# Performance work log

Measured on AMD Instinct MI355X. Metric: run time of the kernel, lower is better.

Reference implementation:

```python
import jax, jax.numpy as jnp
import numpy as np

B, NA, NB, DIM = 1024, 48, 24, 680  # batch, res_alpha(=res_gamma), res_beta, irreps dim = sum_{l<=7}(2l+1)^2


def setup_inputs() -> dict:
    key = jax.random.key(0)
    k1, k2, k3 = jax.random.split(key, 3)
    features = jax.random.normal(k1, (B, DIM), dtype=jnp.float32)
    D = jax.random.normal(k2, (NA, NB, NA, DIM), dtype=jnp.float32)  # stands in for the precomputed Wigner-D buffer
    qw = jax.random.uniform(k3, (NB,), dtype=jnp.float32)  # quadrature weights over beta
    return {"features": features, "D": D, "qw": qw}


def reference(features, D, qw):
    dim = D.shape[-1]
    scale = float(np.sqrt(dim))
    # to_grid: '...i,abci->...abc' / sqrt(dim)
    grid = jnp.einsum('ni,abci->nabc', features, D) / scale  # (B, na, nb, na)
    # from_grid: '...abc,abci,b->...i' * sqrt(dim)  (qw contracts the beta axis)
    out = jnp.einsum('nabc,abci,b->ni', grid, D, qw) * scale  # (B, dim)
    return out
```

## Files before the change

kernel.cpp:

```cpp
#include <hip/hip_runtime.h>
#include <stdint.h>

#define DIM    680
#define DPAD   768
#define NCH    864
#define NB_Q   24
#define SPLITS 36
#define STAGES 24
#define NTILE  6

typedef __bf16 bf16x8 __attribute__((ext_vector_type(8)));
typedef float  f32x16 __attribute__((ext_vector_type(16)));

typedef __attribute__((address_space(3))) unsigned       lds_u32;
typedef __attribute__((address_space(1))) const unsigned glb_u32;

__constant__ int c_tj[NTILE] = {0, 0, 0, 1, 1, 2};
__constant__ int c_ti[NTILE] = {0, 1, 2, 1, 2, 2};

static __device__ __forceinline__ unsigned f2bf(float x) {
    union { float f; unsigned u; } c; c.f = x;
    unsigned u = c.u;
    return (u + 0x7FFFu + ((u >> 16) & 1u)) >> 16;
}

static __device__ __forceinline__ float bf2f(unsigned short h) {
    union { unsigned u; float f; } c; c.u = ((unsigned)h) << 16;
    return c.f;
}

__global__ __launch_bounds__(256) void k1_transpose(
        const float* __restrict__ D, const float* __restrict__ qw,
        uint4* __restrict__ awt) {
    __shared__ float sq[NB_Q];
    __shared__ float tile[4096];
    const int t   = threadIdx.x;
    const int cg0 = blockIdx.x * 4;
    const int i0  = blockIdx.y * 64;
    if (t < NB_Q) sq[t] = sqrtf(qw[t]);

    int  rowr[4], gcol[4];
    bool inb[4];
#pragma unroll
    for (int rd = 0; rd < 4; ++rd) {
        const int row = rd * 16 + (t >> 4);
        const int p   = row >> 3;
        const int sg  = (t & 15) ^ p;
        rowr[rd] = row;
        gcol[rd] = i0 + sg * 4;
        inb[rd]  = (gcol[rd] < DIM);
        if (!inb[rd]) {
            float4 z = {0.f, 0.f, 0.f, 0.f};
            *reinterpret_cast<float4*>(&tile[rd * 1024 + t * 4]) = z;
        }
    }
    __syncthreads();

    for (int cc = 0; cc < 4; ++cc) {
        const int cg = cg0 + cc;
        const int g0 = cg * 64;
#pragma unroll
        for (int rd = 0; rd < 4; ++rd) {
            if (inb[rd]) {
                __builtin_amdgcn_global_load_lds(
                    (glb_u32*)(D + (size_t)(g0 + rowr[rd]) * DIM + gcol[rd]),
                    (lds_u32*)(&tile[rd * 1024 + t * 4]), 16, 0, 0);
            }
        }
        __syncthreads();

#pragma unroll
        for (int s = 0; s < 2; ++s) {
            const int l  = t + s * 256;
            const int c  = l >> 3;
            const int kc = l & 7;
            unsigned h[8];
#pragma unroll
            for (int j = 0; j < 8; ++j) {
                const int row = kc * 8 + j;
                const float v = tile[row * 64 + (((c >> 2) ^ kc) << 2) + (c & 3)];
                const int b = ((g0 + row) / 48) % 24;
                h[j] = f2bf(v * sq[b]);
            }
            uint4 o;
            o.x = h[0] | (h[1] << 16);
            o.y = h[2] | (h[3] << 16);
            o.z = h[4] | (h[5] << 16);
            o.w = h[6] | (h[7] << 16);
            const size_t slot = ((size_t)cg * DPAD + (size_t)(i0 + c)) * 8
                              + (size_t)(kc ^ (c & 7));
            awt[slot] = o;
        }
        __syncthreads();
    }
}

__global__ __launch_bounds__(256) void kf_conv(const float* __restrict__ F,
                                               uint4* __restrict__ Fb) {
    const int idx = blockIdx.x * 256 + threadIdx.x;
    const int row = idx / 96;
    const int c0  = (idx % 96) * 8;
    uint4 o = {0u, 0u, 0u, 0u};
    if (c0 < DIM) {
        const float4 a = *reinterpret_cast<const float4*>(F + (size_t)row * DIM + c0);
        const float4 b = *reinterpret_cast<const float4*>(F + (size_t)row * DIM + c0 + 4);
        o.x = f2bf(a.x) | (f2bf(a.y) << 16);
        o.y = f2bf(a.z) | (f2bf(a.w) << 16);
        o.z = f2bf(b.x) | (f2bf(b.y) << 16);
        o.w = f2bf(b.z) | (f2bf(b.w) << 16);
    }
    Fb[idx] = o;
}

__global__ __launch_bounds__(512) void k2_gram(const uint4* __restrict__ awt,
                                               uint2* __restrict__ parts) {
    __shared__ uint4 smA[2][2048];
    __shared__ uint4 smB[2][2048];
    const int t  = threadIdx.x;
    const int h       = blockIdx.x;
    const int logical = (h & 7) * 27 + (h >> 3);
    const int split   = logical / 6;
    const int t6      = logical % 6;
    const int tj    = c_tj[t6];
    const int ti    = c_ti[t6];
    const bool diag = (tj == ti);
    const int wave  = t >> 6;
    const int lane  = t & 63;
    const int wm    = wave & 3;
    const int wn    = wave >> 2;
    const int cl    = lane & 31;
    const int half  = lane >> 5;

    f32x16 acc[2][4];
    const f32x16 zero = {};
#pragma unroll
    for (int a = 0; a < 2; ++a)
#pragma unroll
        for (int b = 0; b < 4; ++b) acc[a][b] = zero;

#define K2_STAGE(st_, buf_)                                                   \
    do {                                                                      \
        const int    cg_ = split * STAGES + (st_);                            \
        const size_t bA_ = ((size_t)cg_ * DPAD + tj * 256) * 8;               \
        _Pragma("unroll")                                                     \
        for (int j = 0; j < 4; ++j) {                                         \
            __builtin_amdgcn_global_load_lds(                                 \
                (glb_u32*)(awt + bA_ + j * 512 + t),                          \
                (lds_u32*)(&smA[(buf_)][j * 512 + t]), 16, 0, 0);             \
        }                                                                     \
        if (!diag) {                                                          \
            const size_t bB_ = ((size_t)cg_ * DPAD + ti * 256) * 8;           \
            _Pragma("unroll")                                                 \
            for (int j = 0; j < 4; ++j) {                                     \
                __builtin_amdgcn_global_load_lds(                             \
                    (glb_u32*)(awt + bB_ + j * 512 + t),                      \
                    (lds_u32*)(&smB[(buf_)][j * 512 + t]), 16, 0, 0);         \
            }                                                                 \
        }                                                                     \
    } while (0)

    K2_STAGE(0, 0);
    __syncthreads();

    for (int st = 0; st < STAGES; ++st) {
        const int cur = st & 1;
        if (st + 1 < STAGES) K2_STAGE(st + 1, cur ^ 1);

        const bf16x8* pA = reinterpret_cast<const bf16x8*>(smA[cur]);
        const bf16x8* pB = diag ? pA : reinterpret_cast<const bf16x8*>(smB[cur]);
#pragma unroll
        for (int t4 = 0; t4 < 4; ++t4) {
            const int kc = 2 * t4 + half;
            bf16x8 af[2], bfr[4];
#pragma unroll
            for (int ms = 0; ms < 2; ++ms) {
                const int col = wm * 64 + ms * 32 + cl;
                af[ms] = pA[col * 8 + (kc ^ (col & 7))];
            }
#pragma unroll
            for (int ns = 0; ns < 4; ++ns) {
                const int col = wn * 128 + ns * 32 + cl;
                bfr[ns] = pB[col * 8 + (kc ^ (col & 7))];
            }
#pragma unroll
            for (int ms = 0; ms < 2; ++ms)
#pragma unroll
                for (int ns = 0; ns < 4; ++ns)
                    acc[ms][ns] = __builtin_amdgcn_mfma_f32_32x32x16_bf16(
                        af[ms], bfr[ns], acc[ms][ns], 0, 0, 0);
        }
        __syncthreads();
    }
#undef K2_STAGE

    uint2* pt = parts + (size_t)(split * NTILE + t6) * 16384;
#pragma unroll
    for (int ms = 0; ms < 2; ++ms) {
        const int rowb = wm * 64 + ms * 32 + 4 * half;
#pragma unroll
        for (int ns = 0; ns < 4; ++ns) {
            const int colt = wn * 128 + ns * 32 + cl;
#pragma unroll
            for (int q = 0; q < 4; ++q) {
                uint2 w;
                w.x = f2bf(acc[ms][ns][q * 4 + 0]) | (f2bf(acc[ms][ns][q * 4 + 1]) << 16);
                w.y = f2bf(acc[ms][ns][q * 4 + 2]) | (f2bf(acc[ms][ns][q * 4 + 3]) << 16);
                pt[(size_t)(((rowb >> 2) + 2 * q) * 256 + colt)] = w;
            }
        }
    }
}

__global__ __launch_bounds__(256) void k2_reduce(
        const uint2* __restrict__ parts, unsigned short* __restrict__ Mb) {
    const int t6 = blockIdx.y;
    const int tj = c_tj[t6];
    const int ti = c_ti[t6];
    const int idx4 = blockIdx.x * 256 + threadIdx.x;
    const int w0 = idx4 * 2;
    const int quad = w0 >> 8;
    const int c = w0 & 255;
    float s[8] = {0.f, 0.f, 0.f, 0.f, 0.f, 0.f, 0.f, 0.f};
    const uint4* base = reinterpret_cast<const uint4*>(parts) + idx4;
#pragma unroll 4
    for (int sp = 0; sp < SPLITS; ++sp) {
        const uint4 u = base[(size_t)(sp * NTILE + t6) * 8192];
        s[0] += bf2f((unsigned short)(u.x & 0xFFFF));
        s[1] += bf2f((unsigned short)(u.x >> 16));
        s[2] += bf2f((unsigned short)(u.y & 0xFFFF));
        s[3] += bf2f((unsigned short)(u.y >> 16));
        s[4] += bf2f((unsigned short)(u.z & 0xFFFF));
        s[5] += bf2f((unsigned short)(u.z >> 16));
        s[6] += bf2f((unsigned short)(u.w & 0xFFFF));
        s[7] += bf2f((unsigned short)(u.w >> 16));
    }
    const int R = tj * 256 + 4 * quad;
    const int C = ti * 256 + c;
#pragma unroll
    for (int i = 0; i < 4; ++i) {
        const unsigned w = f2bf(s[i]) | (f2bf(s[4 + i]) << 16);
        *reinterpret_cast<unsigned*>(Mb + (size_t)(R + i) * DPAD + C) = w;
    }
    if (ti != tj) {
        uint2 m0, m1;
        m0.x = f2bf(s[0]) | (f2bf(s[1]) << 16);
        m0.y = f2bf(s[2]) | (f2bf(s[3]) << 16);
        m1.x = f2bf(s[4]) | (f2bf(s[5]) << 16);
        m1.y = f2bf(s[6]) | (f2bf(s[7]) << 16);
        *reinterpret_cast<uint2*>(Mb + (size_t)(C + 0) * DPAD + R) = m0;
        *reinterpret_cast<uint2*>(Mb + (size_t)(C + 1) * DPAD + R) = m1;
    }
}

__global__ __launch_bounds__(64) void k3_mfma(const uint4* __restrict__ Fb,
                                              const uint4* __restrict__ Mb,
                                              float* __restrict__ out) {
    __shared__ uint4 sA[2][512];
    __shared__ uint4 sB[2][512];
    const int t    = threadIdx.x;
    const int n0   = blockIdx.x * 64;
    const int i0   = blockIdx.y * 64;
    const int cl   = t & 31;
    const int half = t >> 5;

    f32x16 acc[2][2];
    const f32x16 zero = {};
    acc[0][0] = zero; acc[0][1] = zero; acc[1][0] = zero; acc[1][1] = zero;

#define K3_STAGE(ck_, buf_)                                                   \
    do {                                                                      \
        const int kcs_ = t & 7;                                               \
        _Pragma("unroll")                                                     \
        for (int j = 0; j < 8; ++j) {                                         \
            const int nl_ = j * 8 + (t >> 3);                                 \
            const int sc_ = (ck_) * 8 + (kcs_ ^ (nl_ & 7));                   \
            __builtin_amdgcn_global_load_lds(                                 \
                (glb_u32*)(Fb + (size_t)(n0 + nl_) * 96 + sc_),               \
                (lds_u32*)(&sA[(buf_)][j * 64 + t]), 16, 0, 0);               \
            __builtin_amdgcn_global_load_lds(                                 \
                (glb_u32*)(Mb + (size_t)(i0 + nl_) * 96 + sc_),               \
                (lds_u32*)(&sB[(buf_)][j * 64 + t]), 16, 0, 0);               \
        }                                                                     \
    } while (0)

    K3_STAGE(0, 0);
    asm volatile("s_waitcnt vmcnt(0)" ::: "memory");

    for (int ck = 0; ck < 12; ++ck) {
        const int cur = ck & 1;
        if (ck + 1 < 12) {
            asm volatile("s_waitcnt lgkmcnt(0)" ::: "memory");
            K3_STAGE(ck + 1, cur ^ 1);
            asm volatile("s_waitcnt vmcnt(16)" ::: "memory");
        }
        const bf16x8* pA = reinterpret_cast<const bf16x8*>(sA[cur]);
        const bf16x8* pB = reinterpret_cast<const bf16x8*>(sB[cur]);
#pragma unroll
        for (int t4 = 0; t4 < 4; ++t4) {
            const int kc = 2 * t4 + half;
            bf16x8 af[2], bv[2];
#pragma unroll
            for (int ms = 0; ms < 2; ++ms) {
                const int col = ms * 32 + cl;
                af[ms] = pA[col * 8 + (kc ^ (col & 7))];
            }
#pragma unroll
            for (int ns = 0; ns < 2; ++ns) {
                const int col = ns * 32 + cl;
                bv[ns] = pB[col * 8 + (kc ^ (col & 7))];
            }
#pragma unroll
            for (int ms = 0; ms < 2; ++ms)
#pragma unroll
                for (int ns = 0; ns < 2; ++ns)
                    acc[ms][ns] = __builtin_amdgcn_mfma_f32_32x32x16_bf16(
                        af[ms], bv[ns], acc[ms][ns], 0, 0, 0);
        }
    }
#undef K3_STAGE

#pragma unroll
    for (int ms = 0; ms < 2; ++ms) {
        const int rowb = ms * 32 + 4 * half;
#pragma unroll
        for (int ns = 0; ns < 2; ++ns) {
            const int col = i0 + ns * 32 + cl;
            if (col < DIM) {
#pragma unroll
                for (int q = 0; q < 4; ++q)
#pragma unroll
                    for (int j = 0; j < 4; ++j)
                        out[(size_t)(n0 + rowb + 8 * q + j) * DIM + col]
                            = acc[ms][ns][4 * q + j];
            }
        }
    }
}

extern "C" void kernel_launch(void* const* d_in, const int* in_sizes, int n_in,
                              void* d_out, int out_size, void* d_ws, size_t ws_size,
                              hipStream_t stream) {
    const float* F  = (const float*)d_in[0];
    const float* D  = (const float*)d_in[1];
    const float* qw = (const float*)d_in[2];
    float* out = (float*)d_out;
    char*  ws  = (char*)d_ws;

    uint4* awt = (uint4*)ws;
    const size_t awt_bytes = (size_t)NCH * DPAD * 64 * 2;
    uint2* parts = (uint2*)(ws + awt_bytes);
    const size_t parts_bytes = (size_t)SPLITS * NTILE * 16384 * 8;
    unsigned short* Mb = (unsigned short*)(ws + awt_bytes + parts_bytes);
    const size_t mb_bytes = (size_t)DPAD * DPAD * 2;
    uint4* Fb = (uint4*)(ws + awt_bytes + parts_bytes + mb_bytes);

    k1_transpose<<<dim3(NCH / 4, DPAD / 64), 256, 0, stream>>>(D, qw, awt);
    kf_conv<<<dim3(1024 * DPAD / 8 / 256), 256, 0, stream>>>(F, Fb);
    k2_gram<<<dim3(SPLITS * NTILE), 512, 0, stream>>>(awt, parts);
    k2_reduce<<<dim3(32, NTILE), 256, 0, stream>>>(parts, Mb);
    k3_mfma<<<dim3(16, 11), 64, 0, stream>>>(Fb, (const uint4*)Mb, out);
}
```

Baseline: 303.5 us.

## Double-buffer transpose loads and deepen GEMM prefetch with explicit vmcnt waits

The transpose kernel now uses two LDS tiles, so the global-to-LDS load for the next chunk is issued while the current one is converted, and one barrier per iteration is removed. The GEMM kernel prefetches two stages ahead and replaces __syncthreads with manual s_waitcnt vmcnt counts plus raw s_barrier, so loads stay in flight across iterations. It also raises wave priority around the MFMA block. The hand-tuned vmcnt values must exactly match the number of outstanding loads per stage, so any change to the load count would silently break correctness.

```diff
diff --git a/kernel.cpp b/kernel.cpp
--- a/kernel.cpp
+++ b/kernel.cpp
@@ -33,7 +33,7 @@
         const float* __restrict__ D, const float* __restrict__ qw,
         uint4* __restrict__ awt) {
     __shared__ float sq[NB_Q];
-    __shared__ float tile[4096];
+    __shared__ float tile[2][4096];
     const int t   = threadIdx.x;
     const int cg0 = blockIdx.x * 4;
     const int i0  = blockIdx.y * 64;
@@ -51,23 +51,33 @@
         inb[rd]  = (gcol[rd] < DIM);
         if (!inb[rd]) {
             float4 z = {0.f, 0.f, 0.f, 0.f};
-            *reinterpret_cast<float4*>(&tile[rd * 1024 + t * 4]) = z;
-        }
-    }
+            *reinterpret_cast<float4*>(&tile[0][rd * 1024 + t * 4]) = z;
+            *reinterpret_cast<float4*>(&tile[1][rd * 1024 + t * 4]) = z;
+        }
+    }
+
+#define K1_STAGE(cc_, buf_)                                                   \
+    do {                                                                      \
+        const int g0_ = (cg0 + (cc_)) * 64;                                   \
+        _Pragma("unroll")                                                     \
+        for (int rd = 0; rd < 4; ++rd) {                                      \
+            if (inb[rd]) {                                                    \
+                __builtin_amdgcn_global_load_lds(                             \
+                    (glb_u32*)(D + (size_t)(g0_ + rowr[rd]) * DIM + gcol[rd]),\
+                    (lds_u32*)(&tile[(buf_)][rd * 1024 + t * 4]), 16, 0, 0);  \
+            }                                                                 \
+        }                                                                     \
+    } while (0)
+
     __syncthreads();
+    K1_STAGE(0, 0);
 
     for (int cc = 0; cc < 4; ++cc) {
-        const int cg = cg0 + cc;
-        const int g0 = cg * 64;
-#pragma unroll
-        for (int rd = 0; rd < 4; ++rd) {
-            if (inb[rd]) {
-                __builtin_amdgcn_global_load_lds(
-                    (glb_u32*)(D + (size_t)(g0 + rowr[rd]) * DIM + gcol[rd]),
-                    (lds_u32*)(&tile[rd * 1024 + t * 4]), 16, 0, 0);
-            }
-        }
+        const int cur = cc & 1;
+        const int cg  = cg0 + cc;
+        const int g0  = cg * 64;
         __syncthreads();
+        if (cc + 1 < 4) K1_STAGE(cc + 1, cur ^ 1);
 
 #pragma unroll
         for (int s = 0; s < 2; ++s) {
@@ -78,7 +88,7 @@
 #pragma unroll
             for (int j = 0; j < 8; ++j) {
                 const int row = kc * 8 + j;
-                const float v = tile[row * 64 + (((c >> 2) ^ kc) << 2) + (c & 3)];
+                const float v = tile[cur][row * 64 + (((c >> 2) ^ kc) << 2) + (c & 3)];
                 const int b = ((g0 + row) / 48) % 24;
                 h[j] = f2bf(v * sq[b]);
             }
@@ -91,8 +101,8 @@
                               + (size_t)(kc ^ (c & 7));
             awt[slot] = o;
         }
-        __syncthreads();
-    }
+    }
+#undef K1_STAGE
 }
 
 __global__ __launch_bounds__(256) void kf_conv(const float* __restrict__ F,
@@ -160,11 +170,17 @@
     } while (0)
 
     K2_STAGE(0, 0);
-    __syncthreads();
+    K2_STAGE(1, 1);
 
     for (int st = 0; st < STAGES; ++st) {
         const int cur = st & 1;
-        if (st + 1 < STAGES) K2_STAGE(st + 1, cur ^ 1);
+        if (st + 1 < STAGES) {
+            if (diag) asm volatile("s_waitcnt vmcnt(4)" ::: "memory");
+            else      asm volatile("s_waitcnt vmcnt(8)" ::: "memory");
+        } else {
+            asm volatile("s_waitcnt vmcnt(0)" ::: "memory");
+        }
+        __builtin_amdgcn_s_barrier();
 
         const bf16x8* pA = reinterpret_cast<const bf16x8*>(smA[cur]);
         const bf16x8* pB = diag ? pA : reinterpret_cast<const bf16x8*>(smB[cur]);
@@ -182,14 +198,18 @@
                 const int col = wn * 128 + ns * 32 + cl;
                 bfr[ns] = pB[col * 8 + (kc ^ (col & 7))];
             }
+            __builtin_amdgcn_s_setprio(1);
 #pragma unroll
             for (int ms = 0; ms < 2; ++ms)
 #pragma unroll
                 for (int ns = 0; ns < 4; ++ns)
                     acc[ms][ns] = __builtin_amdgcn_mfma_f32_32x32x16_bf16(
                         af[ms], bfr[ns], acc[ms][ns], 0, 0, 0);
-        }
-        __syncthreads();
+            __builtin_amdgcn_s_setprio(0);
+        }
+        asm volatile("s_waitcnt lgkmcnt(0)" ::: "memory");
+        __builtin_amdgcn_s_barrier();
+        if (st + 2 < STAGES) K2_STAGE(st + 2, cur);
     }
 #undef K2_STAGE
 
```

Measured after the change: 306.9 us. No clear change (+1.1%).

## Fuse D transpose/convert into gram kernel with register-staged prefetch

Applied to the files above, without the earlier changes.

Removes the separate transpose kernel and the bf16 intermediate buffer by having the gram kernel load fp32 D directly into registers, scale by sqrt(qw), convert to bf16 and write swizzled tiles into LDS. Next-stage global loads are issued into registers before the MFMA compute, replacing double-buffered async LDS loads with a single LDS buffer. It also adds s_setprio around the MFMA block. The trade-off is that D is re-read from global memory by several tiles and register pressure increases.

```diff
diff --git a/kernel.cpp b/kernel.cpp
--- a/kernel.cpp
+++ b/kernel.cpp
@@ -3,7 +3,6 @@
 
 #define DIM    680
 #define DPAD   768
-#define NCH    864
 #define NB_Q   24
 #define SPLITS 36
 #define STAGES 24
@@ -29,69 +28,139 @@
     return c.f;
 }
 
-__global__ __launch_bounds__(256) void k1_transpose(
-        const float* __restrict__ D, const float* __restrict__ qw,
-        uint4* __restrict__ awt) {
+__global__ __launch_bounds__(512) void k12_gram(const float* __restrict__ D,
+                                                const float* __restrict__ qw,
+                                                uint2* __restrict__ parts) {
     __shared__ float sq[NB_Q];
-    __shared__ float tile[4096];
-    const int t   = threadIdx.x;
-    const int cg0 = blockIdx.x * 4;
-    const int i0  = blockIdx.y * 64;
+    __shared__ uint4 smA[2048];
+    __shared__ uint4 smB[2048];
+    const int t  = threadIdx.x;
+    const int h       = blockIdx.x;
+    const int logical = (h & 7) * 27 + (h >> 3);
+    const int split   = logical / 6;
+    const int t6      = logical % 6;
+    const int tj    = c_tj[t6];
+    const int ti    = c_ti[t6];
+    const bool diag = (tj == ti);
+    const int cl_ = t & 255;
+    const int hg  = t >> 8;
+    const int cA  = tj * 256 + cl_;
+    const int cB  = ti * 256 + cl_;
+    const bool vA = (cA < DIM);
+    const bool vB = (cB < DIM);
+    const int cAc = vA ? cA : (DIM - 1);
+    const int cBc = vB ? cB : (DIM - 1);
+    const int wave  = t >> 6;
+    const int lane  = t & 63;
+    const int wm    = wave & 3;
+    const int wn    = wave >> 2;
+    const int cl    = lane & 31;
+    const int half  = lane >> 5;
+
+    f32x16 acc[2][4];
+    const f32x16 zero = {};
+#pragma unroll
+    for (int a = 0; a < 2; ++a)
+#pragma unroll
+        for (int b = 0; b < 4; ++b) acc[a][b] = zero;
+
+    float ra[32], rb[32];
+
+#define K12_LOAD(reg_, st_, csrc_)                                            \
+    do {                                                                      \
+        const int g0_ = (split * STAGES + (st_)) * 64 + hg * 32;              \
+        _Pragma("unroll")                                                     \
+        for (int u_ = 0; u_ < 32; ++u_)                                       \
+            reg_[u_] = D[(size_t)(g0_ + u_) * DIM + (csrc_)];                 \
+    } while (0)
+
+#define K12_CONV(reg_, valid_, sm_, st_)                                      \
+    do {                                                                      \
+        const int gg_ = (split * STAGES + (st_)) * 64 + hg * 32;              \
+        _Pragma("unroll")                                                     \
+        for (int kcg_ = 0; kcg_ < 4; ++kcg_) {                                \
+            const int G_ = gg_ + kcg_ * 8;                                    \
+            const int q_ = G_ / 48;                                           \
+            const int r_ = G_ - q_ * 48;                                      \
+            const float s0_ = sq[q_ % 24];                                    \
+            const float s1_ = sq[(q_ + 1) % 24];                              \
+            unsigned hh_[8];                                                  \
+            _Pragma("unroll")                                                 \
+            for (int j_ = 0; j_ < 8; ++j_) {                                  \
+                const float sc_ = (r_ + j_ < 48) ? s0_ : s1_;                 \
+                hh_[j_] = (valid_) ? f2bf(reg_[kcg_ * 8 + j_] * sc_) : 0u;    \
+            }                                                                 \
+            uint4 o_;                                                         \
+            o_.x = hh_[0] | (hh_[1] << 16);                                   \
+            o_.y = hh_[2] | (hh_[3] << 16);                                   \
+            o_.z = hh_[4] | (hh_[5] << 16);                                   \
+            o_.w = hh_[6] | (hh_[7] << 16);                                   \
+            sm_[cl_ * 8 + ((hg * 4 + kcg_) ^ (cl_ & 7))] = o_;                \
+        }                                                                     \
+    } while (0)
+
+    K12_LOAD(ra, 0, cAc);
+    if (!diag) K12_LOAD(rb, 0, cBc);
     if (t < NB_Q) sq[t] = sqrtf(qw[t]);
-
-    int  rowr[4], gcol[4];
-    bool inb[4];
-#pragma unroll
-    for (int rd = 0; rd < 4; ++rd) {
-        const int row = rd * 16 + (t >> 4);
-        const int p   = row >> 3;
-        const int sg  = (t & 15) ^ p;
-        rowr[rd] = row;
-        gcol[rd] = i0 + sg * 4;
-        inb[rd]  = (gcol[rd] < DIM);
-        if (!inb[rd]) {
-            float4 z = {0.f, 0.f, 0.f, 0.f};
-            *reinterpret_cast<float4*>(&tile[rd * 1024 + t * 4]) = z;
-        }
-    }
-    __syncthreads();
-
-    for (int cc = 0; cc < 4; ++cc) {
-        const int cg = cg0 + cc;
-        const int g0 = cg * 64;
-#pragma unroll
-        for (int rd = 0; rd < 4; ++rd) {
-            if (inb[rd]) {
-                __builtin_amdgcn_global_load_lds(
-                    (glb_u32*)(D + (size_t)(g0 + rowr[rd]) * DIM + gcol[rd]),
-                    (lds_u32*)(&tile[rd * 1024 + t * 4]), 16, 0, 0);
-            }
-        }
-        __syncthreads();
-
-#pragma unroll
-        for (int s = 0; s < 2; ++s) {
-            const int l  = t + s * 256;
-            const int c  = l >> 3;
-            const int kc = l & 7;
-            unsigned h[8];
-#pragma unroll
-            for (int j = 0; j < 8; ++j) {
-                const int row = kc * 8 + j;
-                const float v = tile[row * 64 + (((c >> 2) ^ kc) << 2) + (c & 3)];
-                const int b = ((g0 + row) / 48) % 24;
-                h[j] = f2bf(v * sq[b]);
-            }
-            uint4 o;
-            o.x = h[0] | (h[1] << 16);
-            o.y = h[2] | (h[3] << 16);
-            o.z = h[4] | (h[5] << 16);
-            o.w = h[6] | (h[7] << 16);
-            const size_t slot = ((size_t)cg * DPAD + (size_t)(i0 + c)) * 8
-                              + (size_t)(kc ^ (c & 7));
-            awt[slot] = o;
-        }
-        __syncthreads();
+    asm volatile("s_waitcnt lgkmcnt(0)" ::: "memory");
+    __builtin_amdgcn_s_barrier();
+
+    for (int st = 0; st < STAGES; ++st) {
+        K12_CONV(ra, vA, smA, st);
+        if (st + 1 < STAGES) K12_LOAD(ra, st + 1, cAc);
+        if (!diag) {
+            K12_CONV(rb, vB, smB, st);
+            if (st + 1 < STAGES) K12_LOAD(rb, st + 1, cBc);
+        }
+        asm volatile("s_waitcnt lgkmcnt(0)" ::: "memory");
+        __builtin_amdgcn_s_barrier();
+
+        const bf16x8* pA = reinterpret_cast<const bf16x8*>(smA);
+        const bf16x8* pB = diag ? pA : reinterpret_cast<const bf16x8*>(smB);
+#pragma unroll
+        for (int t4 = 0; t4 < 4; ++t4) {
+            const int kc = 2 * t4 + half;
+            bf16x8 af[2], bfr[4];
+#pragma unroll
+            for (int ms = 0; ms < 2; ++ms) {
+                const int col = wm * 64 + ms * 32 + cl;
+                af[ms] = pA[col * 8 + (kc ^ (col & 7))];
+            }
+#pragma unroll
+            for (int ns = 0; ns < 4; ++ns) {
+                const int col = wn * 128 + ns * 32 + cl;
+                bfr[ns] = pB[col * 8 + (kc ^ (col & 7))];
+            }
+            __builtin_amdgcn_s_setprio(1);
+#pragma unroll
+            for (int ms = 0; ms < 2; ++ms)
+#pragma unroll
+                for (int ns = 0; ns < 4; ++ns)
+                    acc[ms][ns] = __builtin_amdgcn_mfma_f32_32x32x16_bf16(
+                        af[ms], bfr[ns], acc[ms][ns], 0, 0, 0);
+            __builtin_amdgcn_s_setprio(0);
+        }
+        asm volatile("s_waitcnt lgkmcnt(0)" ::: "memory");
+        __builtin_amdgcn_s_barrier();
+    }
+#undef K12_LOAD
+#undef K12_CONV
+
+    uint2* pt = parts + (size_t)(split * NTILE + t6) * 16384;
+#pragma unroll
+    for (int ms = 0; ms < 2; ++ms) {
+        const int rowb = wm * 64 + ms * 32 + 4 * half;
+#pragma unroll
+        for (int ns = 0; ns < 4; ++ns) {
+            const int colt = wn * 128 + ns * 32 + cl;
+#pragma unroll
+            for (int q = 0; q < 4; ++q) {
+                uint2 w;
+                w.x = f2bf(acc[ms][ns][q * 4 + 0]) | (f2bf(acc[ms][ns][q * 4 + 1]) << 16);
+                w.y = f2bf(acc[ms][ns][q * 4 + 2]) | (f2bf(acc[ms][ns][q * 4 + 3]) << 16);
+                pt[(size_t)(((rowb >> 2) + 2 * q) * 256 + colt)] = w;
+            }
+        }
     }
 }
 
@@ -110,105 +179,6 @@
         o.w = f2bf(b.z) | (f2bf(b.w) << 16);
     }
     Fb[idx] = o;
-}
-
-__global__ __launch_bounds__(512) void k2_gram(const uint4* __restrict__ awt,
-                                               uint2* __restrict__ parts) {
-    __shared__ uint4 smA[2][2048];
-    __shared__ uint4 smB[2][2048];
-    const int t  = threadIdx.x;
-    const int h       = blockIdx.x;
-    const int logical = (h & 7) * 27 + (h >> 3);
-    const int split   = logical / 6;
-    const int t6      = logical % 6;
-    const int tj    = c_tj[t6];
-    const int ti    = c_ti[t6];
-    const bool diag = (tj == ti);
-    const int wave  = t >> 6;
-    const int lane  = t & 63;
-    const int wm    = wave & 3;
-    const int wn    = wave >> 2;
-    const int cl    = lane & 31;
-    const int half  = lane >> 5;
-
-    f32x16 acc[2][4];
-    const f32x16 zero = {};
-#pragma unroll
-    for (int a = 0; a < 2; ++a)
-#pragma unroll
-        for (int b = 0; b < 4; ++b) acc[a][b] = zero;
-
-#define K2_STAGE(st_, buf_)                                                   \
-    do {                                                                      \
-        const int    cg_ = split * STAGES + (st_);                            \
-        const size_t bA_ = ((size_t)cg_ * DPAD + tj * 256) * 8;               \
-        _Pragma("unroll")                                                     \
-        for (int j = 0; j < 4; ++j) {                                         \
-            __builtin_amdgcn_global_load_lds(                                 \
-                (glb_u32*)(awt + bA_ + j * 512 + t),                          \
-                (lds_u32*)(&smA[(buf_)][j * 512 + t]), 16, 0, 0);             \
-        }                                                                     \
-        if (!diag) {                                                          \
-            const size_t bB_ = ((size_t)cg_ * DPAD + ti * 256) * 8;           \
-            _Pragma("unroll")                                                 \
-            for (int j = 0; j < 4; ++j) {                                     \
-                __builtin_amdgcn_global_load_lds(                             \
-                    (glb_u32*)(awt + bB_ + j * 512 + t),                      \
-                    (lds_u32*)(&smB[(buf_)][j * 512 + t]), 16, 0, 0);         \
-            }                                                                 \
-        }                                                                     \
-    } while (0)
-
-    K2_STAGE(0, 0);
-    __syncthreads();
-
-    for (int st = 0; st < STAGES; ++st) {
-        const int cur = st & 1;
-        if (st + 1 < STAGES) K2_STAGE(st + 1, cur ^ 1);
-
-        const bf16x8* pA = reinterpret_cast<const bf16x8*>(smA[cur]);
-        const bf16x8* pB = diag ? pA : reinterpret_cast<const bf16x8*>(smB[cur]);
-#pragma unroll
-        for (int t4 = 0; t4 < 4; ++t4) {
-            const int kc = 2 * t4 + half;
-            bf16x8 af[2], bfr[4];
-#pragma unroll
-            for (int ms = 0; ms < 2; ++ms) {
-                const int col = wm * 64 + ms * 32 + cl;
-                af[ms] = pA[col * 8 + (kc ^ (col & 7))];
-            }
-#pragma unroll
-            for (int ns = 0; ns < 4; ++ns) {
-                const int col = wn * 128 + ns * 32 + cl;
-                bfr[ns] = pB[col * 8 + (kc ^ (col & 7))];
-            }
-#pragma unroll
-            for (int ms = 0; ms < 2; ++ms)
-#pragma unroll
-                for (int ns = 0; ns < 4; ++ns)
-                    acc[ms][ns] = __builtin_amdgcn_mfma_f32_32x32x16_bf16(
-                        af[ms], bfr[ns], acc[ms][ns], 0, 0, 0);
-        }
-        __syncthreads();
-    }
-#undef K2_STAGE
-
-    uint2* pt = parts + (size_t)(split * NTILE + t6) * 16384;
-#pragma unroll
-    for (int ms = 0; ms < 2; ++ms) {
-        const int rowb = wm * 64 + ms * 32 + 4 * half;
-#pragma unroll
-        for (int ns = 0; ns < 4; ++ns) {
-            const int colt = wn * 128 + ns * 32 + cl;
-#pragma unroll
-            for (int q = 0; q < 4; ++q) {
-                uint2 w;
-                w.x = f2bf(acc[ms][ns][q * 4 + 0]) | (f2bf(acc[ms][ns][q * 4 + 1]) << 16);
-                w.y = f2bf(acc[ms][ns][q * 4 + 2]) | (f2bf(acc[ms][ns][q * 4 + 3]) << 16);
-                pt[(size_t)(((rowb >> 2) + 2 * q) * 256 + colt)] = w;
-            }
-        }
-    }
 }
 
 __global__ __launch_bounds__(256) void k2_reduce(
@@ -346,17 +316,14 @@
     float* out = (float*)d_out;
     char*  ws  = (char*)d_ws;
 
-    uint4* awt = (uint4*)ws;
-    const size_t awt_bytes = (size_t)NCH * DPAD * 64 * 2;
-    uint2* parts = (uint2*)(ws + awt_bytes);
+    uint2* parts = (uint2*)ws;
     const size_t parts_bytes = (size_t)SPLITS * NTILE * 16384 * 8;
-    unsigned short* Mb = (unsigned short*)(ws + awt_bytes + parts_bytes);
+    unsigned short* Mb = (unsigned short*)(ws + parts_bytes);
     const size_t mb_bytes = (size_t)DPAD * DPAD * 2;
-    uint4* Fb = (uint4*)(ws + awt_bytes + parts_bytes + mb_bytes);
-
-    k1_transpose<<<dim3(NCH / 4, DPAD / 64), 256, 0, stream>>>(D, qw, awt);
+    uint4* Fb = (uint4*)(ws + parts_bytes + mb_bytes);
+
+    k12_gram<<<dim3(SPLITS * NTILE), 512, 0, stream>>>(D, qw, parts);
     kf_conv<<<dim3(1024 * DPAD / 8 / 256), 256, 0, stream>>>(F, Fb);
-    k2_gram<<<dim3(SPLITS * NTILE), 512, 0, stream>>>(awt, parts);
     k2_reduce<<<dim3(32, NTILE), 256, 0, stream>>>(parts, Mb);
     k3_mfma<<<dim3(16, 11), 64, 0, stream>>>(Fb, (const uint4*)Mb, out);
 }
```

After: 292.5 us. 1.04x faster.
